# Kernel optimization log

Hardware: AMD Instinct MI355X
Metric: run time of the kernel (lower is better)

## Reference

```python
import jax, jax.numpy as jnp
import numpy as np

# loss hyperparameters (module defaults)
ATTENTION_COEFF = 1.0
GAMMA = 0.5
BETA = 8.0
DICE_COEFF = 2500.0
REV_DICE_COEFF = 2500.0
IOU_COEFF = 0.0
EPS = 1e-14
SMOOTH = 1e-6
LOG_CLAMP = -100.0  # torch F.binary_cross_entropy clamps log terms at -100


def setup_inputs() -> dict:
    key = jax.random.key(0)
    k1, k2 = jax.random.split(key)
    B, C, H, W = 16, 4, 512, 512
    cls_score = jax.random.uniform(k1, (B, C, H, W), dtype=jnp.float32)
    label = jax.random.randint(k2, (B, C, H, W), 0, 2, dtype=jnp.int32)
    return {"cls_score": cls_score, "label": label}


def _attention_bce(pred, t):
    # per-batch alpha = num_neg / total over all 4 channels (vectorized over batch)
    num_pos = jnp.sum(t, axis=(1, 2, 3))                      # (B,)
    total = jnp.float32(t.shape[1] * t.shape[2] * t.shape[3])
    alpha = ((total - num_pos) / total)[:, None, None, None]  # (B,1,1,1)
    p_clip = jnp.clip(pred, EPS, 1.0 - EPS)
    # beta ** ((1-p)**gamma) and beta ** (p**gamma)
    w = (t * alpha * BETA ** ((1.0 - p_clip) ** GAMMA)
         + (1.0 - t) * (1.0 - alpha) * BETA ** (p_clip ** GAMMA))
    w = jax.lax.stop_gradient(w)
    # BCE on raw pred, with torch-style log clamping
    log_p = jnp.maximum(jnp.log(pred), LOG_CLAMP)
    log_1mp = jnp.maximum(jnp.log(1.0 - pred), LOG_CLAMP)
    bce = -(t * log_p + (1.0 - t) * log_1mp)
    return jnp.sum(w * bce)


def _dice(pred, t):
    inter = jnp.sum(pred * t, axis=(2, 3))                    # (B,4)
    denom = jnp.sum(pred * pred, axis=(2, 3)) + jnp.sum(t * t, axis=(2, 3))
    return jnp.sum(1.0 - (2.0 * inter + SMOOTH) / (denom + SMOOTH))


def _iou(pred, t):
    inter = jnp.sum(pred * t, axis=(2, 3))
    union = jnp.sum(pred + t, axis=(2, 3)) - inter
    return jnp.sum(1.0 - (inter + SMOOTH) / (union + SMOOTH))


def reference(cls_score, label):
    t = label.astype(jnp.float32)  # (B,4,H,W)
    loss = ATTENTION_COEFF * _attention_bce(cls_score, t)
    loss = loss + DICE_COEFF * _dice(cls_score, t)
    loss = loss + REV_DICE_COEFF * _dice(1.0 - cls_score, 1.0 - t)
    loss = loss + IOU_COEFF * _iou(cls_score, t)
    return loss
```

## Files before the change

### kernel.cpp

```cpp
#include <hip/hip_runtime.h>
#include <hip/hip_bf16.h>


#define B_DIM 16
#define C_DIM 4
#define HW 262144
#define NPLANES 64
#define K_CHUNKS 32
#define CHUNK (HW / K_CHUNKS)
#define NBLOCKS (NPLANES * K_CHUNKS)
#define NSUMS 6
#define NITER (CHUNK / 4 / 256)

__global__ __launch_bounds__(256, 6) void loss_main(
    const float* __restrict__ pred, const int* __restrict__ label,
    float* __restrict__ ws) {
  const int block = blockIdx.x;
  const int plane = block >> 5;
  const int chunk = block & (K_CHUNKS - 1);
  const long base = (long)plane * HW + (long)chunk * CHUNK;
  const float4* p4 = (const float4*)(pred + base);
  const int4*   t4 = (const int4*)(label + base);
  const int tid = threadIdx.x;

  float s_pt = 0.f, s_pp = 0.f, s_p = 0.f;
  float nsum_t = 0.f;
  float nsum_1 = 0.f;
  int   s_ti = 0;

  float4 P[NITER];
  int4   T[NITER];
#pragma unroll
  for (int it = 0; it < NITER; ++it) {
    P[it] = p4[tid + it * 256];
    T[it] = t4[tid + it * 256];
  }

#pragma unroll
  for (int it = 0; it < NITER; ++it) {
    float pe[4] = {P[it].x, P[it].y, P[it].z, P[it].w};
    int   te[4] = {T[it].x, T[it].y, T[it].z, T[it].w};
#pragma unroll
    for (int j = 0; j < 4; ++j) {
      float pv = pe[j];
      float tf = (float)te[j];
      float u   = __builtin_fmaf(tf, -2.0f, 1.0f);
      float arg = __builtin_fmaf(pv, u, tf);
      float x   = 1.0f - arg;
      float r  = __builtin_amdgcn_sqrtf(x);
      float Bw = __builtin_amdgcn_exp2f(3.0f * r);
      float lg = __builtin_amdgcn_logf(arg);
      float L  = fmaxf(0.69314718056f * lg, -100.0f);
      float c  = Bw * (-L);
      nsum_t += c;
      nsum_1 = __builtin_fmaf(tf, c, nsum_1);
      s_pt   = __builtin_fmaf(tf, pv, s_pt);
      s_pp   = __builtin_fmaf(pv, pv, s_pp);
      s_p   += pv;
      s_ti  += te[j];
    }
  }

  float s_t = (float)s_ti;

  float vals[NSUMS] = {s_pt, s_pp, s_t, s_p, nsum_1, nsum_t};
  __shared__ float lds[4][NSUMS];
#pragma unroll
  for (int q = 0; q < NSUMS; ++q) {
    float v = vals[q];
#pragma unroll
    for (int off = 32; off; off >>= 1) v += __shfl_down(v, off);
    vals[q] = v;
  }
  const int wave = tid >> 6;
  if ((tid & 63) == 0) {
#pragma unroll
    for (int q = 0; q < NSUMS; ++q) lds[wave][q] = vals[q];
  }
  __syncthreads();
  if (tid < NSUMS) {
    float v = lds[0][tid] + lds[1][tid] + lds[2][tid] + lds[3][tid];
    ws[block * NSUMS + tid] = v;
  }
}

__global__ __launch_bounds__(64) void loss_finalize(
    const float* __restrict__ ws, float* __restrict__ out) {
  const int p = threadIdx.x;
  float s[NSUMS] = {0.f, 0.f, 0.f, 0.f, 0.f, 0.f};
  for (int k = 0; k < K_CHUNKS; ++k) {
    const float* w = ws + (p * K_CHUNKS + k) * NSUMS;
#pragma unroll
    for (int q = 0; q < NSUMS; ++q) s[q] += w[q];
  }
  const float s_pt = s[0], s_pp = s[1], s_t = s[2], s_p = s[3];
  const float sum1 = s[4];
  const float sum2 = s[5] - s[4];
  const float N = (float)HW;
  const float SM = 1e-6f;

  float dice = 1.0f - (2.0f * s_pt + SM) / (s_pp + s_t + SM);
  float inter2 = N - s_p - s_t + s_pt;
  float denom2 = 2.0f * N - 2.0f * s_p + s_pp - s_t;
  float rdice = 1.0f - (2.0f * inter2 + SM) / (denom2 + SM);

  float np4 = s_t + __shfl_xor(s_t, 1);
  np4 += __shfl_xor(np4, 2);
  const float total = (float)(C_DIM * HW);
  float alpha = (total - np4) / total;

  float val = alpha * sum1 + (1.0f - alpha) * sum2
            + 2500.0f * (dice + rdice);

#pragma unroll
  for (int off = 32; off; off >>= 1) val += __shfl_down(val, off);
  if (p == 0) out[0] = val;
}

extern "C" void kernel_launch(void* const* d_in, const int* in_sizes, int n_in,
                              void* d_out, int out_size, void* d_ws, size_t ws_size,
                              hipStream_t stream) {
  const float* pred = (const float*)d_in[0];
  const int* label = (const int*)d_in[1];
  float* out = (float*)d_out;
  float* ws = (float*)d_ws;

  loss_main<<<NBLOCKS, 256, 0, stream>>>(pred, label, ws);
  loss_finalize<<<1, 64, 0, stream>>>(ws, out);
}
```

Before: 28.22 us.

## Stage inputs through LDS with direct global-to-LDS loads, use 512-thread blocks

Replaces register-held vector global loads with per-wave global_load_lds transfers that write the chunk straight into shared memory. Each block then reads float4/int4 values from LDS for the compute and reductions. Block size doubles to 512 threads, so each thread handles fewer elements. This aims to raise the number of memory requests in flight without register pressure, at the cost of 64 KB of LDS per block, which limits occupancy, plus a barrier before compute.

```diff
diff --git a/kernel.cpp b/kernel.cpp
--- a/kernel.cpp
+++ b/kernel.cpp
@@ -1,6 +1,8 @@
 #include <hip/hip_runtime.h>
-#include <hip/hip_bf16.h>
 
+
+typedef float f32x4 __attribute__((ext_vector_type(4)));
+typedef int   i32x4 __attribute__((ext_vector_type(4)));
 
 #define B_DIM 16
 #define C_DIM 4
@@ -10,61 +12,71 @@
 #define CHUNK (HW / K_CHUNKS)
 #define NBLOCKS (NPLANES * K_CHUNKS)
 #define NSUMS 6
-#define NITER (CHUNK / 4 / 256)
+#define NTHREADS 512
+#define NWAVES (NTHREADS / 64)
+#define WELEMS (CHUNK / NWAVES)
+#define WOPS (WELEMS / 256)
 
-__global__ __launch_bounds__(256, 6) void loss_main(
+__global__ __launch_bounds__(NTHREADS) void loss_main(
     const float* __restrict__ pred, const int* __restrict__ label,
     float* __restrict__ ws) {
+  __shared__ float sp[NWAVES][WELEMS];
+  __shared__ int   st[NWAVES][WELEMS];
+  __shared__ float red[NWAVES][NSUMS];
+
   const int block = blockIdx.x;
   const int plane = block >> 5;
   const int chunk = block & (K_CHUNKS - 1);
-  const long base = (long)plane * HW + (long)chunk * CHUNK;
-  const float4* p4 = (const float4*)(pred + base);
-  const int4*   t4 = (const int4*)(label + base);
   const int tid = threadIdx.x;
+  const int w = tid >> 6, l = tid & 63;
+  const long wbase = (long)plane * HW + (long)chunk * CHUNK + (long)w * WELEMS;
+  const float* gp = pred + wbase;
+  const int*   gt = label + wbase;
+
+#pragma unroll
+  for (int r = 0; r < WOPS; ++r) {
+    __builtin_amdgcn_global_load_lds(
+        (const __attribute__((address_space(1))) void*)(gp + r * 256 + l * 4),
+        (__attribute__((address_space(3))) void*)(&sp[w][r * 256]), 16, 0, 0);
+    __builtin_amdgcn_global_load_lds(
+        (const __attribute__((address_space(1))) void*)(gt + r * 256 + l * 4),
+        (__attribute__((address_space(3))) void*)(&st[w][r * 256]), 16, 0, 0);
+  }
+  __syncthreads();
 
   float s_pt = 0.f, s_pp = 0.f, s_p = 0.f;
   float nsum_t = 0.f;
   float nsum_1 = 0.f;
   int   s_ti = 0;
 
-  float4 P[NITER];
-  int4   T[NITER];
 #pragma unroll
-  for (int it = 0; it < NITER; ++it) {
-    P[it] = p4[tid + it * 256];
-    T[it] = t4[tid + it * 256];
-  }
-
-#pragma unroll
-  for (int it = 0; it < NITER; ++it) {
-    float pe[4] = {P[it].x, P[it].y, P[it].z, P[it].w};
-    int   te[4] = {T[it].x, T[it].y, T[it].z, T[it].w};
+  for (int r = 0; r < WOPS; ++r) {
+    f32x4 P = *(const f32x4*)&sp[w][r * 256 + l * 4];
+    i32x4 T = *(const i32x4*)&st[w][r * 256 + l * 4];
 #pragma unroll
     for (int j = 0; j < 4; ++j) {
-      float pv = pe[j];
-      float tf = (float)te[j];
+      float pv = P[j];
+      float tf = (float)T[j];
       float u   = __builtin_fmaf(tf, -2.0f, 1.0f);
       float arg = __builtin_fmaf(pv, u, tf);
       float x   = 1.0f - arg;
-      float r  = __builtin_amdgcn_sqrtf(x);
-      float Bw = __builtin_amdgcn_exp2f(3.0f * r);
-      float lg = __builtin_amdgcn_logf(arg);
-      float L  = fmaxf(0.69314718056f * lg, -100.0f);
-      float c  = Bw * (-L);
+      float r_  = __builtin_amdgcn_sqrtf(x);
+      float Bw  = __builtin_amdgcn_exp2f(3.0f * r_);
+      float lg  = __builtin_amdgcn_logf(arg);
+      float L   = fmaxf(0.69314718056f * lg, -100.0f);
+      float c   = Bw * (-L);
       nsum_t += c;
-      nsum_1 = __builtin_fmaf(tf, c, nsum_1);
-      s_pt   = __builtin_fmaf(tf, pv, s_pt);
-      s_pp   = __builtin_fmaf(pv, pv, s_pp);
-      s_p   += pv;
-      s_ti  += te[j];
+      nsum_1  = __builtin_fmaf(tf, c, nsum_1);
+      s_pt    = __builtin_fmaf(tf, pv, s_pt);
+      s_pp    = __builtin_fmaf(pv, pv, s_pp);
+      s_p    += pv;
+      s_ti   += T[j];
     }
   }
 
   float s_t = (float)s_ti;
 
   float vals[NSUMS] = {s_pt, s_pp, s_t, s_p, nsum_1, nsum_t};
-  __shared__ float lds[4][NSUMS];
 #pragma unroll
   for (int q = 0; q < NSUMS; ++q) {
     float v = vals[q];
@@ -72,14 +84,15 @@
     for (int off = 32; off; off >>= 1) v += __shfl_down(v, off);
     vals[q] = v;
   }
-  const int wave = tid >> 6;
-  if ((tid & 63) == 0) {
+  if (l == 0) {
 #pragma unroll
-    for (int q = 0; q < NSUMS; ++q) lds[wave][q] = vals[q];
+    for (int q = 0; q < NSUMS; ++q) red[w][q] = vals[q];
   }
   __syncthreads();
   if (tid < NSUMS) {
-    float v = lds[0][tid] + lds[1][tid] + lds[2][tid] + lds[3][tid];
+    float v = 0.f;
+#pragma unroll
+    for (int ww = 0; ww < NWAVES; ++ww) v += red[ww][tid];
     ws[block * NSUMS + tid] = v;
   }
 }
@@ -125,6 +138,6 @@
   float* out = (float*)d_out;
   float* ws = (float*)d_ws;
 
-  loss_main<<<NBLOCKS, 256, 0, stream>>>(pred, label, ws);
+  loss_main<<<NBLOCKS, NTHREADS, 0, stream>>>(pred, label, ws);
   loss_finalize<<<1, 64, 0, stream>>>(ws, out);
 }
```

New measurement: 30.54 us. 1.08x slower.
